# Kernel tuning notes

Measured on AMD Instinct MI355X. Metric: run time of the kernel, lower is better.

## Reference

```python
import jax, jax.numpy as jnp
import numpy as np

SIZE, NC, BITS = 16, 3, 8
NV = NC * BITS * SIZE * SIZE  # 6144
NH = NV
N = 32
K_LS = 32   # fixed cap on T=0 local-search Gibbs sweeps (converged rows are fixed points)
K_CP = 16   # fixed cap on coupling MH iterations (converged rows masked out)


def float2bit(x, bits=BITS):
    # quantize [0,1) floats to `bits` binary planes, as in float2bit(...).flatten(1)
    q = jnp.clip(jnp.floor(x * (2 ** bits)), 0, 2 ** bits - 1).astype(jnp.int32)
    shifts = jnp.arange(bits, dtype=jnp.int32)
    b = (q[..., None] >> shifts) & 1  # [N,nc,H,W,bits]
    return b.astype(jnp.float32)


def energy(params, v, h0, h1):
    W0, W1, b0, b1, b2 = params
    e = -jnp.sum(v * b0, axis=1)
    e = e - jnp.sum(h0 * (v @ W0.T + b1), axis=1)
    e = e - jnp.sum(h1 * (h0 @ W1.T + b2), axis=1)
    return e


def _samp(logits, r, T):
    if T == 0:
        return (logits >= 0).astype(jnp.float32)
    return (r < jax.nn.sigmoid(logits / T)).astype(jnp.float32)


def gibbs_step(params, v, h0, h1, even, fix_v, T, key):
    W0, W1, b0, b1, b2 = params
    if T == 0:
        rv = rh0 = rh1 = None
    else:
        kv, k0, k1 = jax.random.split(key, 3)
        rv = jax.random.uniform(kv, v.shape)
        rh0 = jax.random.uniform(k0, h0.shape)
        rh1 = jax.random.uniform(k1, h1.shape)
    # 'even' sweep order: v -> odd h layers -> even h layers
    v_e = v if fix_v else _samp(h0 @ W0 + b0, rv, T)
    h1_e = _samp(h0 @ W1.T + b2, rh1, T)
    h0_e = _samp(v_e @ W0.T + b1 + h1_e @ W1, rh0, T)
    # 'odd' sweep order: even h layers -> v -> odd h layers
    h0_o = _samp(v @ W0.T + b1 + h1 @ W1, rh0, T)
    v_o = v if fix_v else _samp(h0_o @ W0 + b0, rv, T)
    h1_o = _samp(h0_o @ W1.T + b2, rh1, T)
    m = even[:, None]
    return (jnp.where(m, v_e, v_o), jnp.where(m, h0_e, h0_o), jnp.where(m, h1_e, h1_o))


def local_search(params, v, h0, h1, fix_v, key):
    # T=0 deterministic descent with a fixed per-row even/odd split (rand_u drawn once);
    # converged rows are fixed points of the map, so running a fixed K_LS sweeps over the
    # full batch is equivalent to the torch masked while-loop (up to the iteration cap).
    even = jax.random.uniform(key, (v.shape[0],)) < 0.5
    def body(i, s):
        return gibbs_step(params, s[0], s[1], s[2], even, fix_v, 0, None)
    return jax.lax.fori_loop(0, K_LS, body, (v, h0, h1))


def mh_step(params, v, h0, h1, fix_v, key):
    kv, k0, k1, ku = jax.random.split(key, 4)
    v_p = v if fix_v else (jax.random.uniform(kv, v.shape) < 0.5).astype(jnp.float32)
    h0_p = (jax.random.uniform(k0, h0.shape) < 0.5).astype(jnp.float32)
    h1_p = (jax.random.uniform(k1, h1.shape) < 0.5).astype(jnp.float32)
    log_ratio = energy(params, v, h0, h1) - energy(params, v_p, h0_p, h1_p)
    acc = jax.random.uniform(ku, (v.shape[0],)) < jnp.exp(jnp.minimum(log_ratio, 0.0))
    a = acc[:, None]
    return (v if fix_v else jnp.where(a, v_p, v), jnp.where(a, h0_p, h0), jnp.where(a, h1_p, h1))


def _conv_mask(v_new, h0_new, h1_new, v, h0, h1, fix_v):
    c = jnp.ones(v.shape[0], bool) if fix_v else jnp.all(v_new == v, axis=1)
    return c & jnp.all(h0_new == h0, axis=1) & jnp.all(h1_new == h1, axis=1)


def coupling(params, v, h0, h1, fix_v, key):
    k0, key = jax.random.split(key)
    v1, h01, h11 = mh_step(params, v, h0, h1, fix_v, k0)
    e = energy(params, v1, h01, h11)
    conv = _conv_mask(v1, h01, h11, v, h0, h1, fix_v)
    def body(state, k):
        v, h0, h1, e, conv = state
        v2, h02, h12 = mh_step(params, v, h0, h1, fix_v, k)
        de = energy(params, v2, h02, h12) - energy(params, v, h0, h1)
        m = ~conv
        e = e + jnp.where(m, de, 0.0)
        conv2 = _conv_mask(v2, h02, h12, v, h0, h1, fix_v)
        mm = m[:, None]
        v = jnp.where(mm, v2, v)
        h0 = jnp.where(mm, h02, h0)
        h1 = jnp.where(mm, h12, h1)
        return (v, h0, h1, e, conv | conv2), None
    keys = jax.random.split(key, K_CP)
    (v, h0, h1, e, conv), _ = jax.lax.scan(body, (v1, h01, h11, e, conv), keys)
    return e, v, h0, h1


def _dbm_loss(v_img, W0, W1, b0, b1, b2):
    params = (W0, W1, b0, b1, b2)
    n = v_img.shape[0]
    ks = jax.random.split(jax.random.key(42), 13)
    v = float2bit(v_img).reshape(n, -1)
    # positive phase (visibles clamped, fix_v=True)
    h0 = (jax.random.uniform(ks[0], (n, NH)) < 0.5).astype(jnp.float32)
    h1 = (jax.random.uniform(ks[1], (n, NH)) < 0.5).astype(jnp.float32)
    v, h0, h1 = local_search(params, v, h0, h1, True, ks[2])
    even = jax.random.uniform(ks[3], (n,)) < 0.5
    v, h0, h1 = gibbs_step(params, v, h0, h1, even, True, 1, ks[4])
    e_pos, v, h0, h1 = coupling(params, v, h0, h1, True, ks[5])
    # negative phase (free-running)
    v = (jax.random.uniform(ks[6], v.shape) < 0.5).astype(jnp.float32)
    h0 = (jax.random.uniform(ks[7], (n, NH)) < 0.5).astype(jnp.float32)
    h1 = (jax.random.uniform(ks[8], (n, NH)) < 0.5).astype(jnp.float32)
    v, h0, h1 = local_search(params, v, h0, h1, False, ks[9])
    even = jax.random.uniform(ks[10], (n,)) < 0.5
    v, h0, h1 = gibbs_step(params, v, h0, h1, even, False, 1, ks[11])
    e_neg, v, h0, h1 = coupling(params, v, h0, h1, False, ks[12])
    return e_pos - e_neg  # [N]


def setup_inputs() -> dict:
    key = jax.random.key(0)
    kv, kw0, kw1 = jax.random.split(key, 3)
    v = jax.random.uniform(kv, (N, NC, SIZE, SIZE), dtype=jnp.float32)
    # orthogonal-like scale (unit-norm rows): entries ~ 1/sqrt(fan_in)
    W0 = jax.random.normal(kw0, (NH, NV), dtype=jnp.float32) / np.sqrt(NV)
    W1 = jax.random.normal(kw1, (NH, NH), dtype=jnp.float32) / np.sqrt(NH)
    b0 = jnp.zeros((NV,), jnp.float32)
    b1 = jnp.zeros((NH,), jnp.float32)
    b2 = jnp.zeros((NH,), jnp.float32)
    return {"v": v, "W0": W0, "W1": W1, "b0": b0, "b1": b1, "b2": b2}


def reference(v, W0, W1, b0, b1, b2):
    return _dbm_loss(v, W0, W1, b0, b1, b2)
```

## Files before the change

kernel.cpp:

```cpp
#include <hip/hip_runtime.h>
#include <cstdint>
#include <math.h>

typedef unsigned int u32;
typedef unsigned long long u64;
typedef double d4 __attribute__((ext_vector_type(4)));

#define TF_PARTITIONABLE 1

#define NU 6144
#define NB 32
#define NTOT (NU * NB)
#define NWORD 96
#define NCH 16
#define CHK 384
#define NT_TILES 12
#define HALF_BIG 98304u
#define HALF_SMALL 16u

struct Key { u32 a, b; };
struct UVec { float u[NB]; };

__host__ __device__ __forceinline__ void tf2x32(u32 k0, u32 k1, u32 x0, u32 x1, u32& o0, u32& o1) {
  const u32 k2 = k0 ^ k1 ^ 0x1BD11BDAu;
#define TFR(r) { x0 += x1; x1 = (x1 << r) | (x1 >> (32 - r)); x1 ^= x0; }
  x0 += k0; x1 += k1;
  TFR(13) TFR(15) TFR(26) TFR(6)  x0 += k1; x1 += k2 + 1u;
  TFR(17) TFR(29) TFR(16) TFR(24) x0 += k2; x1 += k0 + 2u;
  TFR(13) TFR(15) TFR(26) TFR(6)  x0 += k0; x1 += k1 + 3u;
  TFR(17) TFR(29) TFR(16) TFR(24) x0 += k1; x1 += k2 + 4u;
  TFR(13) TFR(15) TFR(26) TFR(6)  x0 += k2; x1 += k0 + 5u;
#undef TFR
  o0 = x0; o1 = x1;
}

__host__ __device__ __forceinline__ u32 rbits(u32 k0, u32 k1, u32 t, u32 half) {
#if TF_PARTITIONABLE
  (void)half;
  u32 a, b; tf2x32(k0, k1, 0u, t, a, b); return a ^ b;
#else
  u32 a, b;
  if (t < half) { tf2x32(k0, k1, t, half + t, a, b); return a; }
  tf2x32(k0, k1, t - half, t, a, b); return b;
#endif
}

__host__ __device__ __forceinline__ float u01f(u32 bits) {
  union { u32 u; float f; } c; c.u = (bits >> 9) | 0x3f800000u;
  return c.f - 1.0f;
}

__device__ __forceinline__ double pav(int probe, int l) {
  return probe ? (double)(((l * 13 + 5) & 63) + 1) : (double)(l + 1);
}
__device__ __forceinline__ double pbv(int probe, int l) {
  return probe ? (double)(((l * 11 + 2) & 63) + 1) : (double)(((l * 7 + 3) & 63) + 1);
}

__global__ __launch_bounds__(64) void k_calib(int* __restrict__ tbl) {
  int L = threadIdx.x;
  d4 z = {0.0, 0.0, 0.0, 0.0};
  d4 o0 = __builtin_amdgcn_mfma_f64_16x16x4f64(pav(0, L), pbv(0, L), z, 0, 0, 0);
  d4 o1 = __builtin_amdgcn_mfma_f64_16x16x4f64(pav(1, L), pbv(1, L), z, 0, 0, 0);
  int q = L >> 4, m16 = L & 15;
  int best = -1;
  for (int combo = 0; combo < 16; ++combo) {
    int fa = combo & 1, fb = (combo >> 1) & 1, fd = combo >> 2;
    int ok = 1;
    for (int probe = 0; probe < 2; ++probe) {
#pragma unroll
      for (int r = 0; r < 4; ++r) {
        int i, j;
        if (fd == 0)      { j = m16; i = 4 * q + r; }
        else if (fd == 1) { j = m16; i = q + 4 * r; }
        else if (fd == 2) { i = m16; j = 4 * q + r; }
        else              { i = m16; j = q + 4 * r; }
        double pred = 0.0;
#pragma unroll
        for (int k = 0; k < 4; ++k) {
          int la = fa ? (i * 4 + k) : (k * 16 + i);
          int lb = fb ? (j * 4 + k) : (k * 16 + j);
          pred += pav(probe, la) * pbv(probe, lb);
        }
        double obs = probe ? (r == 0 ? o1[0] : r == 1 ? o1[1] : r == 2 ? o1[2] : o1[3])
                           : (r == 0 ? o0[0] : r == 1 ? o0[1] : r == 2 ? o0[2] : o0[3]);
        if (pred != obs) ok = 0;
      }
    }
    if (__all(ok) && best < 0) best = combo;
  }
  int mA = 0, kA = 0, nB = 0, kB = 0, b0_ = 0, bs = 0, j0 = 0, js = 0, okf = 0;
  if (best >= 0) {
    int fa = best & 1, fb = (best >> 1) & 1, fd = best >> 2;
    if (fa) { mA = L >> 2; kA = L & 3; } else { mA = m16; kA = q; }
    if (fb) { nB = L >> 2; kB = L & 3; } else { nB = m16; kB = q; }
    if (fd == 0)      { j0 = m16; js = 0; b0_ = 4 * q; bs = 1; }
    else if (fd == 1) { j0 = m16; js = 0; b0_ = q; bs = 4; }
    else if (fd == 2) { b0_ = m16; bs = 0; j0 = 4 * q; js = 1; }
    else              { b0_ = m16; bs = 0; j0 = q; js = 4; }
    okf = 1;
  }
  int* p = tbl + L * 16;
  p[0] = mA; p[1] = kA; p[2] = nB; p[3] = kB;
  p[4] = b0_; p[5] = bs; p[6] = j0; p[7] = js; p[8] = okf;
}

__global__ void k_init(u32* __restrict__ flag, u32* __restrict__ chg) { *flag = 0u; *chg = 0u; }

__global__ void k_conv(u32* __restrict__ flag, u32* __restrict__ chg) {
  if (*flag == 0u && *chg == 0u) *flag = 1u;
  *chg = 0u;
}

__global__ void k_allconv(const u32* __restrict__ conv, u32* __restrict__ skipc) {
  if (*skipc) return;
  u32 all = 1u;
  for (int b = 0; b < NB; ++b) all &= conv[b];
  if (all) *skipc = 1u;
}

__global__ __launch_bounds__(256) void k_pos_v(const float* __restrict__ vin, u64* __restrict__ pk) {
  int tid = blockIdx.x * 256 + threadIdx.x;
  int b = tid / 768, p = tid % 768;
  float x = vin[tid];
  int q = (int)floorf(x * 256.0f);
  q = q < 0 ? 0 : (q > 255 ? 255 : q);
  ((unsigned char*)pk)[b * 768 + p] = (unsigned char)q;
}

__global__ __launch_bounds__(256) void k_bern(u32 k0, u32 k1, u64* __restrict__ pk) {
  int tid = blockIdx.x * 256 + threadIdx.x;
  bool s = u01f(rbits(k0, k1, (u32)tid, HALF_BIG)) < 0.5f;
  u64 m = __ballot(s);
  if ((threadIdx.x & 63) == 0) pk[tid >> 6] = m;
}

__global__ __launch_bounds__(256) void k_bern3(u32 has_v, u32 va, u32 vb, u32 ha0, u32 hb0,
                                               u32 ha1, u32 hb1,
                                               u64* __restrict__ pkv, u64* __restrict__ pkh0,
                                               u64* __restrict__ pkh1, const u32* __restrict__ skip) {
  if (skip && *skip) return;
  int tid = blockIdx.x * 256 + threadIdx.x;
  int lane0 = (threadIdx.x & 63) == 0;
  if (has_v) {
    bool s = u01f(rbits(va, vb, (u32)tid, HALF_BIG)) < 0.5f;
    u64 m = __ballot(s);
    if (lane0) pkv[tid >> 6] = m;
  }
  { bool s = u01f(rbits(ha0, hb0, (u32)tid, HALF_BIG)) < 0.5f;
    u64 m = __ballot(s);
    if (lane0) pkh0[tid >> 6] = m; }
  { bool s = u01f(rbits(ha1, hb1, (u32)tid, HALF_BIG)) < 0.5f;
    u64 m = __ballot(s);
    if (lane0) pkh1[tid >> 6] = m; }
}

__device__ __forceinline__ bool samp_dec(float f, int t1, u32 k0, u32 k1, u32 tid) {
  if (t1) {
    double u = (double)u01f(rbits(k0, k1, tid, HALF_BIG));
    return u < 1.0 / (1.0 + exp(-(double)f));
  }
  return f >= 0.0f;
}

__global__ __launch_bounds__(256) void k_samp(const float* __restrict__ fE, const float* __restrict__ fO,
                                              u32 even, int t1, u32 k0, u32 k1,
                                              u64* __restrict__ pk,
                                              const u32* __restrict__ skip, u32* __restrict__ chg) {
  if (skip && *skip) return;
  int tid = blockIdx.x * 256 + threadIdx.x;
  int b = tid / NU;
  float f = ((even >> b) & 1u) ? fE[tid] : fO[tid];
  bool s = samp_dec(f, t1, k0, k1, (u32)tid);
  u64 m = __ballot(s);
  if ((threadIdx.x & 63) == 0) {
    int widx = tid >> 6;
    if (chg) { u64 old = pk[widx]; if (old != m) *chg = 1u; }
    pk[widx] = m;
  }
}

__global__ __launch_bounds__(256) void k_gemm_n(const float* __restrict__ W, const u64* __restrict__ pkx,
                                                double* __restrict__ part, const u32* __restrict__ skip,
                                                const int* __restrict__ tbl) {
  if (skip && *skip) return;
  __shared__ double smem_d[2560];
  int jt = blockIdx.x % 96, c = blockIdx.x / 96;
  int wid = threadIdx.x >> 6, lane = threadIdx.x & 63;
  int kbase = c * CHK;
  int jn0 = jt * 64;
  const int* tp = tbl + lane * 16;
  int okf = tp[8];
  if (okf) {
    float* lw = (float*)smem_d;
    int mA = tp[0], kA = tp[1], nB = tp[2], kB = tp[3];
    int bD0 = tp[4], bDs = tp[5], jD0 = tp[6], jDs = tp[7];
    int t256 = threadIdx.x;
    d4 acc0 = {0.0, 0.0, 0.0, 0.0};
    d4 acc1 = {0.0, 0.0, 0.0, 0.0};
#pragma unroll
    for (int r = 0; r < 2; ++r) {
      int idx = r * 256 + t256, kk = idx >> 4, qq = idx & 15;
      float4 w4 = *(const float4*)(W + (size_t)(kbase + kk) * NU + jn0 + 4 * qq);
      float* d = &lw[kk * 80 + 4 * qq];
      d[0] = w4.x; d[1] = w4.y; d[2] = w4.z; d[3] = w4.w;
    }
    __syncthreads();
    const u64* pxr0 = pkx + (size_t)mA * NWORD + (kbase >> 6);
    const u64* pxr1 = pkx + (size_t)(mA + 16) * NWORD + (kbase >> 6);
    int buf = 0;
    for (int t = 0; t < NT_TILES; ++t) {
      float4 w0p, w1p;
      bool pf = (t + 1) < NT_TILES;
      if (pf) {
        int k0n = kbase + (t + 1) * 32;
        { int idx = t256,       kk = idx >> 4, qq = idx & 15;
          w0p = *(const float4*)(W + (size_t)(k0n + kk) * NU + jn0 + 4 * qq); }
        { int idx = 256 + t256, kk = idx >> 4, qq = idx & 15;
          w1p = *(const float4*)(W + (size_t)(k0n + kk) * NU + jn0 + 4 * qq); }
      }
      u64 ww0 = pxr0[t >> 1], ww1 = pxr1[t >> 1];
      u32 sh = ((u32)(t & 1) << 5) + (u32)kA;
      u32 bb0 = (u32)(ww0 >> sh), bb1 = (u32)(ww1 >> sh);
      const float* lwp = &lw[(buf * 32 + kB) * 80 + wid * 16 + nB];
#pragma unroll
      for (int u = 0; u < 8; ++u) {
        double a0 = (double)((bb0 >> (4 * u)) & 1u);
        double a1 = (double)((bb1 >> (4 * u)) & 1u);
        double wv = (double)lwp[320 * u];
        acc0 = __builtin_amdgcn_mfma_f64_16x16x4f64(a0, wv, acc0, 0, 0, 0);
        acc1 = __builtin_amdgcn_mfma_f64_16x16x4f64(a1, wv, acc1, 0, 0, 0);
      }
      if (pf) {
        int nb = buf ^ 1;
        { int idx = t256,       kk = idx >> 4, qq = idx & 15;
          float* d = &lw[(nb * 32 + kk) * 80 + 4 * qq];
          d[0] = w0p.x; d[1] = w0p.y; d[2] = w0p.z; d[3] = w0p.w; }
        { int idx = 256 + t256, kk = idx >> 4, qq = idx & 15;
          float* d = &lw[(nb * 32 + kk) * 80 + 4 * qq];
          d[0] = w1p.x; d[1] = w1p.y; d[2] = w1p.z; d[3] = w1p.w; }
      }
      __syncthreads();
      buf ^= 1;
    }
    int jn = jn0 + wid * 16;
    double* pp = part + (size_t)c * NTOT + jn;
#pragma unroll
    for (int r = 0; r < 4; ++r) {
      int bi = bD0 + bDs * r, jj = jD0 + jDs * r;
      pp[(size_t)bi * NU + jj] = acc0[r];
      pp[(size_t)(bi + 16) * NU + jj] = acc1[r];
    }
  } else {
    double* red = smem_d;
    int j = jn0 + lane;
    int i0 = kbase + wid * (CHK / 4);
    const float* wp = W + (size_t)i0 * NU + j;
    double acc[32];
#pragma unroll
    for (int b = 0; b < 32; ++b) acc[b] = 0.0;
    for (int i = 0; i < CHK / 4; ++i) {
      double w = (double)wp[(size_t)i * NU];
      int k = i0 + i;
#pragma unroll
      for (int b = 0; b < 32; ++b) {
        double xb = (double)((pkx[(size_t)b * NWORD + (k >> 6)] >> (k & 63)) & 1ull);
        acc[b] = fma(xb, w, acc[b]);
      }
    }
    for (int w = 1; w < 4; ++w) {
      if (wid == w) {
#pragma unroll
        for (int b = 0; b < 32; ++b) red[b * 64 + lane] = acc[b];
      }
      __syncthreads();
      if (wid == 0) {
#pragma unroll
        for (int b = 0; b < 32; ++b) acc[b] += red[b * 64 + lane];
      }
      __syncthreads();
    }
    if (wid == 0) {
      double* pp = part + (size_t)c * NTOT + j;
#pragma unroll
      for (int b = 0; b < 32; ++b) pp[(size_t)b * NU] = acc[b];
    }
  }
}

__global__ __launch_bounds__(256) void k_gemm_t(const float* __restrict__ W, const u64* __restrict__ pkx,
                                                double* __restrict__ part, const u32* __restrict__ skip,
                                                const int* __restrict__ tbl) {
  if (skip && *skip) return;
  __shared__ double smem_d[2176];
  int jt = blockIdx.x % 96, c = blockIdx.x / 96;
  int wid = threadIdx.x >> 6, lane = threadIdx.x & 63;
  int kbase = c * CHK;
  int jn0 = jt * 64;
  const int* tp = tbl + lane * 16;
  int okf = tp[8];
  if (okf) {
    float* lw = (float*)smem_d;
    int mA = tp[0], kA = tp[1], nB = tp[2], kB = tp[3];
    int bD0 = tp[4], bDs = tp[5], jD0 = tp[6], jDs = tp[7];
    int t256 = threadIdx.x;
    d4 acc0 = {0.0, 0.0, 0.0, 0.0};
    d4 acc1 = {0.0, 0.0, 0.0, 0.0};
#pragma unroll
    for (int r = 0; r < 2; ++r) {
      int idx = r * 256 + t256, jj = idx >> 3, kq = idx & 7;
      float4 w4 = *(const float4*)(W + (size_t)(jn0 + jj) * NU + kbase + 4 * kq);
      float* d = &lw[jj * 34 + 4 * kq];
      d[0] = w4.x; d[1] = w4.y; d[2] = w4.z; d[3] = w4.w;
    }
    __syncthreads();
    const u64* pxr0 = pkx + (size_t)mA * NWORD + (kbase >> 6);
    const u64* pxr1 = pkx + (size_t)(mA + 16) * NWORD + (kbase >> 6);
    int buf = 0;
    for (int t = 0; t < NT_TILES; ++t) {
      float4 w0p, w1p;
      bool pf = (t + 1) < NT_TILES;
      if (pf) {
        int k0n = kbase + (t + 1) * 32;
        { int idx = t256,       jj = idx >> 3, kq = idx & 7;
          w0p = *(const float4*)(W + (size_t)(jn0 + jj) * NU + k0n + 4 * kq); }
        { int idx = 256 + t256, jj = idx >> 3, kq = idx & 7;
          w1p = *(const float4*)(W + (size_t)(jn0 + jj) * NU + k0n + 4 * kq); }
      }
      u64 ww0 = pxr0[t >> 1], ww1 = pxr1[t >> 1];
      u32 sh = ((u32)(t & 1) << 5) + (u32)kA;
      u32 bb0 = (u32)(ww0 >> sh), bb1 = (u32)(ww1 >> sh);
      const float* lwp = &lw[(buf * 64 + wid * 16 + nB) * 34 + kB];
#pragma unroll
      for (int u = 0; u < 8; ++u) {
        double a0 = (double)((bb0 >> (4 * u)) & 1u);
        double a1 = (double)((bb1 >> (4 * u)) & 1u);
        double wv = (double)lwp[4 * u];
        acc0 = __builtin_amdgcn_mfma_f64_16x16x4f64(a0, wv, acc0, 0, 0, 0);
        acc1 = __builtin_amdgcn_mfma_f64_16x16x4f64(a1, wv, acc1, 0, 0, 0);
      }
      if (pf) {
        int nb = buf ^ 1;
        { int idx = t256,       jj = idx >> 3, kq = idx & 7;
          float* d = &lw[(nb * 64 + jj) * 34 + 4 * kq];
          d[0] = w0p.x; d[1] = w0p.y; d[2] = w0p.z; d[3] = w0p.w; }
        { int idx = 256 + t256, jj = idx >> 3, kq = idx & 7;
          float* d = &lw[(nb * 64 + jj) * 34 + 4 * kq];
          d[0] = w1p.x; d[1] = w1p.y; d[2] = w1p.z; d[3] = w1p.w; }
      }
      __syncthreads();
      buf ^= 1;
    }
    int jn = jn0 + wid * 16;
    double* pp = part + (size_t)c * NTOT + jn;
#pragma unroll
    for (int r = 0; r < 4; ++r) {
      int bi = bD0 + bDs * r, jj = jD0 + jDs * r;
      pp[(size_t)bi * NU + jj] = acc0[r];
      pp[(size_t)(bi + 16) * NU + jj] = acc1[r];
    }
  } else {
    float* lwf = (float*)smem_d;
    double* red = smem_d;
    int qf = threadIdx.x & 7, af = threadIdx.x >> 3;
    double acc[32];
#pragma unroll
    for (int b = 0; b < 32; ++b) acc[b] = 0.0;
    for (int s = 0; s < NT_TILES; ++s) {
      int ib = kbase + s * 32;
#pragma unroll
      for (int pass = 0; pass < 2; ++pass) {
        int r = pass * 32 + af;
        float4 w4 = *(const float4*)(W + (size_t)(jn0 + r) * NU + ib + qf * 4);
        lwf[(qf * 4 + 0) * 65 + r] = w4.x;
        lwf[(qf * 4 + 1) * 65 + r] = w4.y;
        lwf[(qf * 4 + 2) * 65 + r] = w4.z;
        lwf[(qf * 4 + 3) * 65 + r] = w4.w;
      }
      __syncthreads();
      int iw = wid * 8;
      for (int ii = 0; ii < 8; ++ii) {
        double w = (double)lwf[(iw + ii) * 65 + lane];
        int k = ib + iw + ii;
#pragma unroll
        for (int b = 0; b < 32; ++b) {
          double xb = (double)((pkx[(size_t)b * NWORD + (k >> 6)] >> (k & 63)) & 1ull);
          acc[b] = fma(xb, w, acc[b]);
        }
      }
      __syncthreads();
    }
    for (int w = 1; w < 4; ++w) {
      if (wid == w) {
#pragma unroll
        for (int b = 0; b < 32; ++b) red[b * 64 + lane] = acc[b];
      }
      __syncthreads();
      if (wid == 0) {
#pragma unroll
        for (int b = 0; b < 32; ++b) acc[b] += red[b * 64 + lane];
      }
      __syncthreads();
    }
    if (wid == 0) {
      double* pp = part + (size_t)c * NTOT + jn0 + lane;
#pragma unroll
      for (int b = 0; b < 32; ++b) pp[(size_t)b * NU] = acc[b];
    }
  }
}

__global__ __launch_bounds__(256) void k_reduce(const double* __restrict__ part, const float* __restrict__ bias,
                                                const float* __restrict__ src, float* __restrict__ out,
                                                const u32* __restrict__ skip) {
  if (skip && *skip) return;
  int tid = blockIdx.x * 256 + threadIdx.x;
  int j = tid % NU;
  double s = src ? (double)src[tid] : 0.0;
  if (bias) s += (double)bias[j];
#pragma unroll
  for (int c = 0; c < NCH; ++c) s += part[(size_t)c * NTOT + tid];
  out[tid] = (float)s;
}

__global__ __launch_bounds__(256) void k_redsamp(const double* __restrict__ part, const float* __restrict__ bias,
                                                 const float* __restrict__ src, float* __restrict__ out,
                                                 int t1, u32 k0, u32 k1,
                                                 u64* __restrict__ pk,
                                                 const u32* __restrict__ skip, u32 wmask,
                                                 u32* __restrict__ chg) {
  if (skip && *skip) return;
  int tid = blockIdx.x * 256 + threadIdx.x;
  int j = tid % NU, b = tid / NU;
  double s = src ? (double)src[tid] : 0.0;
  if (bias) s += (double)bias[j];
#pragma unroll
  for (int c = 0; c < NCH; ++c) s += part[(size_t)c * NTOT + tid];
  float f = (float)s;
  if (out) out[tid] = f;
  bool wr = (wmask >> b) & 1u;
  bool smp = samp_dec(f, t1, k0, k1, (u32)tid);
  u64 m = __ballot(smp);
  if (((threadIdx.x & 63) == 0) && wr) {
    int widx = tid >> 6;
    if (chg) { u64 old = pk[widx]; if (old != m) *chg = 1u; }
    pk[widx] = m;
  }
  (void)j;
}

__global__ __launch_bounds__(256) void k_energy(const u64* __restrict__ pkv, const u64* __restrict__ pkh0,
                                                const u64* __restrict__ pkh1, const float* __restrict__ f1,
                                                const float* __restrict__ f2, const float* __restrict__ b0,
                                                float* __restrict__ eout, const u32* __restrict__ skip) {
  if (skip && *skip) return;
  __shared__ double red[256];
  int b = blockIdx.x, t = threadIdx.x;
  double s = 0.0;
  for (int j = t; j < NU; j += 256) {
    int w = j >> 6, bit = j & 63;
    if ((pkv [b * NWORD + w] >> bit) & 1ull) s += (double)b0[j];
    if ((pkh0[b * NWORD + w] >> bit) & 1ull) s += (double)f1[(size_t)b * NU + j];
    if ((pkh1[b * NWORD + w] >> bit) & 1ull) s += (double)f2[(size_t)b * NU + j];
  }
  red[t] = s; __syncthreads();
  for (int off = 128; off > 0; off >>= 1) { if (t < off) red[t] += red[t + off]; __syncthreads(); }
  if (t == 0) eout[b] = (float)(-red[0]);
}

__global__ __launch_bounds__(64) void k_accept(float* __restrict__ ecur, const float* __restrict__ eprop,
                                               float* __restrict__ erun, u32* __restrict__ conv,
                                               u32* __restrict__ accf,
                                               const u64* __restrict__ pv, const u64* __restrict__ pcv,
                                               const u64* __restrict__ ph0, const u64* __restrict__ pch0,
                                               const u64* __restrict__ ph1, const u64* __restrict__ pch1,
                                               UVec uv, int first, const u32* __restrict__ skip) {
  if (skip && *skip) return;
  int b = blockIdx.x, t = threadIdx.x;
  u64 diff = 0ull;
  for (int w = t; w < NWORD; w += 64) {
    size_t o = (size_t)b * NWORD + w;
    if (pv) diff |= pv[o] ^ pcv[o];
    diff |= ph0[o] ^ pch0[o];
    diff |= ph1[o] ^ pch1[o];
  }
  int neq = __any(diff != 0ull);
  if (t == 0) {
    float ec = ecur[b], ep = eprop[b];
    bool acc = (double)uv.u[b] < exp(fmin((double)ec - (double)ep, 0.0));
    bool m = first ? true : (conv[b] == 0u);
    bool upd = m && acc;
    if (first) erun[b] = acc ? ep : ec;
    else if (upd) erun[b] += (ep - ec);
    if (upd) ecur[b] = ep;
    u32 c2 = acc ? (neq ? 0u : 1u) : 1u;
    conv[b] = first ? c2 : (conv[b] | c2);
    accf[b] = upd ? 1u : 0u;
  }
}

__global__ __launch_bounds__(256) void k_merge_pk(const u32* __restrict__ accf,
                                                  const u64* __restrict__ pa, u64* __restrict__ ca,
                                                  const u64* __restrict__ pb, u64* __restrict__ cb,
                                                  const u64* __restrict__ pc, u64* __restrict__ cc,
                                                  const u32* __restrict__ skip) {
  if (skip && *skip) return;
  int w = blockIdx.x * 256 + threadIdx.x;
  if (w >= NB * NWORD) return;
  int b = w / NWORD;
  if (accf[b]) {
    ca[w] = pa[w];
    cb[w] = pb[w];
    if (pc) cc[w] = pc[w];
  }
}

__global__ void k_final(const float* __restrict__ ep, const float* __restrict__ en, float* __restrict__ out) {
  int b = threadIdx.x;
  if (b < NB) out[b] = ep[b] - en[b];
}

static void split_keys(Key k, int n, Key* out) {
#if TF_PARTITIONABLE
  for (int i = 0; i < n; ++i) { u32 a, b; tf2x32(k.a, k.b, 0u, (u32)i, a, b); out[i].a = a; out[i].b = b; }
#else
  u32 flat[64];
  for (int i = 0; i < n; ++i) { u32 a, b; tf2x32(k.a, k.b, (u32)i, (u32)(n + i), a, b); flat[i] = a; flat[n + i] = b; }
  for (int i = 0; i < n; ++i) { out[i].a = flat[2 * i]; out[i].b = flat[2 * i + 1]; }
#endif
}
static u32 mask32(Key k) {
  u32 m = 0;
  for (int b = 0; b < NB; ++b)
    if (u01f(rbits(k.a, k.b, (u32)b, HALF_SMALL)) < 0.5f) m |= (1u << b);
  return m;
}

extern "C" void kernel_launch(void* const* d_in, const int* in_sizes, int n_in,
                              void* d_out, int out_size, void* d_ws, size_t ws_size,
                              hipStream_t stream) {
  const float* vin = (const float*)d_in[0];
  const float* W0  = (const float*)d_in[1];
  const float* W1  = (const float*)d_in[2];
  const float* b0  = (const float*)d_in[3];
  const float* b1  = (const float*)d_in[4];
  const float* b2  = (const float*)d_in[5];
  float* outp = (float*)d_out;

  char* ws = (char*)d_ws;
  size_t off = 0;
  auto alloc = [&](size_t bytes) -> void* {
    void* p = ws + off; off += (bytes + 255) & ~(size_t)255; return p;
  };
  enum { SV = 0, SH0, SH1, SVE, SH1E, SH0O, SVP, SH0P, SH1P, NS };
  enum { IV = 0, IA, IB, IC, ID, IE, IF2, NF };
  u64* PK[NS]; float* F[NF];
  for (int f = 0; f < NF; ++f) F[f] = (float*)alloc((size_t)NTOT * 4);
  double* PART = (double*)alloc((size_t)NCH * NTOT * 8);
  for (int s = 0; s < NS; ++s) PK[s] = (u64*)alloc((size_t)NB * NWORD * 8);
  int*   TBL    = (int*)alloc(64 * 16 * 4);
  float* E_CUR  = (float*)alloc(256);
  float* E_PROP = (float*)alloc(256);
  float* E_POS  = (float*)alloc(256);
  float* E_NEG  = (float*)alloc(256);
  u32*   ACC    = (u32*)alloc(256);
  u32*   CONV   = (u32*)alloc(256);
  u32*   FLAG   = (u32*)alloc(256);
  u32*   CHG    = (u32*)alloc(256);
  u32*   SKIPC  = (u32*)alloc(256);
  u32*   DUMMY  = (u32*)alloc(256);
  if (off > ws_size) return;

  Key root{0u, 42u};
  Key ks[13]; split_keys(root, 13, ks);
  const Key KZ{0u, 0u};

  k_calib<<<dim3(1), dim3(64), 0, stream>>>(TBL);

  auto GEMM_T = [&](const float* Wm, int xs, const u32* skip) {
    k_gemm_t<<<dim3(96 * NCH), dim3(256), 0, stream>>>(Wm, PK[xs], PART, skip, TBL);
  };
  auto GEMM_N = [&](const float* Wm, int xs, const u32* skip) {
    k_gemm_n<<<dim3(96 * NCH), dim3(256), 0, stream>>>(Wm, PK[xs], PART, skip, TBL);
  };
  auto RED = [&](const float* bias, const float* src, float* dst, const u32* skip) {
    k_reduce<<<dim3(768), dim3(256), 0, stream>>>(PART, bias, src, dst, skip);
  };
  auto REDS = [&](const float* bias, const float* src, float* dst, int t1, Key k, int sdst,
                  const u32* skip, u32 wm, u32* chg) {
    k_redsamp<<<dim3(768), dim3(256), 0, stream>>>(PART, bias, src, dst, t1, k.a, k.b,
                                                   PK[sdst], skip, wm, chg);
  };
  auto GT = [&](const float* Wm, int xs, const float* bias, const float* src, float* dst, const u32* skip) {
    GEMM_T(Wm, xs, skip); RED(bias, src, dst, skip);
  };
  auto GN = [&](const float* Wm, int xs, const float* bias, const float* src, float* dst, const u32* skip) {
    GEMM_N(Wm, xs, skip); RED(bias, src, dst, skip);
  };
  auto GTS = [&](const float* Wm, int xs, const float* bias, const float* src, float* dst,
                 int t1, Key k, int sdst, const u32* skip) {
    GEMM_T(Wm, xs, skip); REDS(bias, src, dst, t1, k, sdst, skip, ~0u, nullptr);
  };
  auto GNS = [&](const float* Wm, int xs, const float* bias, const float* src, float* dst,
                 int t1, Key k, int sdst, const u32* skip) {
    GEMM_N(Wm, xs, skip); REDS(bias, src, dst, t1, k, sdst, skip, ~0u, nullptr);
  };
  auto SAMP = [&](const float* fE, const float* fO, u32 even, int t1, Key k, int dst,
                  const u32* skip, u32* chg) {
    k_samp<<<dim3(768), dim3(256), 0, stream>>>(fE, fO, even, t1, k.a, k.b, PK[dst], skip, chg);
  };
  auto BERN = [&](Key k, int dst) {
    k_bern<<<dim3(768), dim3(256), 0, stream>>>(k.a, k.b, PK[dst]);
  };
  auto ENERGY = [&](int sv, int sh0, int sh1, const float* f1, const float* f2, float* eo, const u32* skip) {
    k_energy<<<dim3(32), dim3(256), 0, stream>>>(PK[sv], PK[sh0], PK[sh1], f1, f2, b0, eo, skip);
  };

  auto ls_fixv = [&](u32 evm) {
    auto X = [&](u32 wm) {
      GEMM_T(W1, SH0, FLAG);
      REDS(b2, nullptr, nullptr, 0, KZ, SH1, FLAG, wm, CHG);
    };
    auto Y = [&]() {
      GEMM_N(W1, SH1, FLAG);
      REDS(nullptr, F[IV], nullptr, 0, KZ, SH0, FLAG, ~0u, CHG);
    };
    k_init<<<dim3(1), dim3(1), 0, stream>>>(FLAG, CHG);
    X(evm);
    for (int i = 0; i < 31; ++i) {
      Y(); X(~0u);
      k_conv<<<dim3(1), dim3(1), 0, stream>>>(FLAG, CHG);
    }
    Y(); X(~evm);
  };
  auto ls_free = [&](u32 evm) {
    auto X = [&](u32 wm) {
      GEMM_N(W0, SH0, FLAG);
      REDS(b0, nullptr, nullptr, 0, KZ, SV, FLAG, wm, CHG);
      GEMM_T(W1, SH0, FLAG);
      REDS(b2, nullptr, nullptr, 0, KZ, SH1, FLAG, wm, CHG);
    };
    auto Y = [&]() {
      GT(W0, SV, b1, nullptr, F[IC], FLAG);
      GEMM_N(W1, SH1, FLAG);
      REDS(nullptr, F[IC], nullptr, 0, KZ, SH0, FLAG, ~0u, CHG);
    };
    k_init<<<dim3(1), dim3(1), 0, stream>>>(FLAG, CHG);
    X(evm);
    for (int i = 0; i < 31; ++i) {
      Y(); X(~0u);
      k_conv<<<dim3(1), dim3(1), 0, stream>>>(FLAG, CHG);
    }
    Y(); X(~evm);
  };

  auto gibbs_fixv = [&](u32 even, Key kh0, Key kh1) {
    GTS(W1, SH0, b2, nullptr, F[IA], 1, kh1, SH1E, nullptr);
    GN(W1, SH1E, nullptr, F[IV], F[IB], nullptr);
    GNS(W1, SH1, nullptr, F[IV], F[IC], 1, kh0, SH0O, nullptr);
    GT(W1, SH0O, b2, nullptr, F[ID], nullptr);
    SAMP(F[IB], F[IC], even, 1, kh0, SH0, nullptr, nullptr);
    SAMP(F[IA], F[ID], even, 1, kh1, SH1, nullptr, nullptr);
  };
  auto gibbs_free = [&](u32 even, Key kv, Key kh0, Key kh1) {
    GNS(W0, SH0, b0, nullptr, F[IE], 1, kv, SVE, nullptr);
    GTS(W1, SH0, b2, nullptr, F[IA], 1, kh1, SH1E, nullptr);
    GT(W0, SVE, b1, nullptr, F[IB], nullptr);
    GN(W1, SH1E, nullptr, F[IB], F[IB], nullptr);
    GT(W0, SV, b1, nullptr, F[IC], nullptr);
    GNS(W1, SH1, nullptr, F[IC], F[IC], 1, kh0, SH0O, nullptr);
    GN(W0, SH0O, b0, nullptr, F[IF2], nullptr);
    GT(W1, SH0O, b2, nullptr, F[ID], nullptr);
    SAMP(F[IE], F[IF2], even, 1, kv, SV, nullptr, nullptr);
    SAMP(F[IB], F[IC], even, 1, kh0, SH0, nullptr, nullptr);
    SAMP(F[IA], F[ID], even, 1, kh1, SH1, nullptr, nullptr);
  };

  auto coupling = [&](bool fixv, Key ck, float* erun) {
    Key top[2]; split_keys(ck, 2, top);
    Key cks[17]; cks[0] = top[0];
    { Key rest[16]; split_keys(top[1], 16, rest); for (int i = 0; i < 16; ++i) cks[i + 1] = rest[i]; }
    k_init<<<dim3(1), dim3(1), 0, stream>>>(SKIPC, DUMMY);
    for (int it = 0; it < 17; ++it) {
      const u32* sk = (it == 0) ? nullptr : SKIPC;
      Key sub[4]; split_keys(cks[it], 4, sub);
      UVec uv;
      for (int b = 0; b < NB; ++b) uv.u[b] = u01f(rbits(sub[3].a, sub[3].b, (u32)b, HALF_SMALL));
      k_bern3<<<dim3(768), dim3(256), 0, stream>>>(fixv ? 0u : 1u,
          sub[0].a, sub[0].b, sub[1].a, sub[1].b, sub[2].a, sub[2].b,
          PK[SVP], PK[SH0P], PK[SH1P], sk);
      const float* f1;
      if (fixv) f1 = F[IV];
      else { GT(W0, SVP, b1, nullptr, F[IC], sk); f1 = F[IC]; }
      GT(W1, SH0P, b2, nullptr, F[ID], sk);
      ENERGY(fixv ? SV : SVP, SH0P, SH1P, f1, F[ID], E_PROP, sk);
      k_accept<<<dim3(32), dim3(64), 0, stream>>>(E_CUR, E_PROP, erun, CONV, ACC,
          fixv ? nullptr : PK[SVP], fixv ? nullptr : PK[SV],
          PK[SH0P], PK[SH0], PK[SH1P], PK[SH1], uv, it == 0 ? 1 : 0, sk);
      k_merge_pk<<<dim3(12), dim3(256), 0, stream>>>(ACC, PK[SH0P], PK[SH0], PK[SH1P], PK[SH1],
          fixv ? nullptr : PK[SVP], fixv ? nullptr : PK[SV], sk);
      k_allconv<<<dim3(1), dim3(1), 0, stream>>>(CONV, SKIPC);
    }
  };

  k_pos_v<<<dim3(96), dim3(256), 0, stream>>>(vin, PK[SV]);
  BERN(ks[0], SH0);
  BERN(ks[1], SH1);
  GT(W0, SV, b1, nullptr, F[IV], nullptr);
  u32 ev_ls_pos = mask32(ks[2]);
  ls_fixv(ev_ls_pos);
  u32 ev2_pos = mask32(ks[3]);
  Key g4[3]; split_keys(ks[4], 3, g4);
  gibbs_fixv(ev2_pos, g4[1], g4[2]);
  GT(W1, SH0, b2, nullptr, F[ID], nullptr);
  ENERGY(SV, SH0, SH1, F[IV], F[ID], E_CUR, nullptr);
  coupling(true, ks[5], E_POS);

  BERN(ks[6], SV);
  BERN(ks[7], SH0);
  BERN(ks[8], SH1);
  u32 ev_ls_neg = mask32(ks[9]);
  ls_free(ev_ls_neg);
  u32 ev2_neg = mask32(ks[10]);
  Key g11[3]; split_keys(ks[11], 3, g11);
  gibbs_free(ev2_neg, g11[0], g11[1], g11[2]);
  GT(W0, SV, b1, nullptr, F[IB], nullptr);
  GT(W1, SH0, b2, nullptr, F[IA], nullptr);
  ENERGY(SV, SH0, SH1, F[IB], F[IA], E_CUR, nullptr);
  coupling(false, ks[12], E_NEG);

  k_final<<<dim3(1), dim3(64), 0, stream>>>(E_POS, E_NEG, outp);
}
```

Measured before the change: 13.50 ms.

## Detect period-2 cycles in local search and split fallback GEMM batch accumulators

The local-search loop's convergence test is reworked. Instead of tracking per-write changes with atomics-style flags in the sampling kernels, a new kernel snapshots the packed states into alternating save slots after each sweep. When a state repeats two sweeps later, the loop is treated as having reached a fixed point or 2-cycle, and the remaining sweeps are skipped. A fixup kernel restores the correct parity state so the result matches running every iteration. Separately, the fallback GEMM paths accumulate 8 batch rows at a time in four groups instead of 32 at once, which lowers register pressure at the cost of re-reading the weights four times.

```diff
diff --git a/kernel.cpp b/kernel.cpp
--- a/kernel.cpp
+++ b/kernel.cpp
@@ -12,6 +12,7 @@
 #define NB 32
 #define NTOT (NU * NB)
 #define NWORD 96
+#define SW (NB * NWORD)
 #define NCH 16
 #define CHK 384
 #define NT_TILES 12
@@ -105,18 +106,49 @@
   p[4] = b0_; p[5] = bs; p[6] = j0; p[7] = js; p[8] = okf;
 }
 
-__global__ void k_init(u32* __restrict__ flag, u32* __restrict__ chg) { *flag = 0u; *chg = 0u; }
-
-__global__ void k_conv(u32* __restrict__ flag, u32* __restrict__ chg) {
-  if (*flag == 0u && *chg == 0u) *flag = 1u;
-  *chg = 0u;
-}
+__global__ void k_init(u32* __restrict__ a, u32* __restrict__ b) { *a = 0u; *b = 0u; }
 
 __global__ void k_allconv(const u32* __restrict__ conv, u32* __restrict__ skipc) {
   if (*skipc) return;
   u32 all = 1u;
   for (int b = 0; b < NB; ++b) all &= conv[b];
   if (all) *skipc = 1u;
+}
+
+__global__ __launch_bounds__(256) void k_cyc(const u64* __restrict__ s0, const u64* __restrict__ s1,
+                                             const u64* __restrict__ s2, u64* __restrict__ save,
+                                             int slot, int docmp, int rem_odd, int prev_slot,
+                                             u32* __restrict__ flag, u32* __restrict__ fix) {
+  if (*flag) return;
+  __shared__ u32 neq_sh;
+  if (threadIdx.x == 0) neq_sh = 0u;
+  __syncthreads();
+  u64* sp = save + (size_t)slot * (3 * SW);
+  u32 neq = 0;
+  for (int w = threadIdx.x; w < SW; w += 256) {
+    u64 a0 = s0[w]; if (a0 != sp[w]) neq = 1; sp[w] = a0;
+    u64 a1 = s1[w]; if (a1 != sp[SW + w]) neq = 1; sp[SW + w] = a1;
+    if (s2) { u64 a2 = s2[w]; if (a2 != sp[2 * SW + w]) neq = 1; sp[2 * SW + w] = a2; }
+  }
+  if (neq) neq_sh = 1u;
+  __syncthreads();
+  if (threadIdx.x == 0 && docmp && neq_sh == 0u) {
+    *flag = 1u;
+    *fix = rem_odd ? (1u + (u32)prev_slot) : 0u;
+  }
+}
+
+__global__ __launch_bounds__(256) void k_fixup(u64* __restrict__ s0, u64* __restrict__ s1,
+                                               u64* __restrict__ s2, const u64* __restrict__ save,
+                                               const u32* __restrict__ flag, const u32* __restrict__ fix) {
+  if (!*flag || !*fix) return;
+  const u64* sp = save + (size_t)(*fix - 1u) * (3 * SW);
+  int w = blockIdx.x * 256 + threadIdx.x;
+  if (w < SW) {
+    s0[w] = sp[w];
+    s1[w] = sp[SW + w];
+    if (s2) s2[w] = sp[2 * SW + w];
+  }
 }
 
 __global__ __launch_bounds__(256) void k_pos_v(const float* __restrict__ vin, u64* __restrict__ pk) {
@@ -165,19 +197,14 @@
 
 __global__ __launch_bounds__(256) void k_samp(const float* __restrict__ fE, const float* __restrict__ fO,
                                               u32 even, int t1, u32 k0, u32 k1,
-                                              u64* __restrict__ pk,
-                                              const u32* __restrict__ skip, u32* __restrict__ chg) {
+                                              u64* __restrict__ pk, const u32* __restrict__ skip) {
   if (skip && *skip) return;
   int tid = blockIdx.x * 256 + threadIdx.x;
   int b = tid / NU;
   float f = ((even >> b) & 1u) ? fE[tid] : fO[tid];
   bool s = samp_dec(f, t1, k0, k1, (u32)tid);
   u64 m = __ballot(s);
-  if ((threadIdx.x & 63) == 0) {
-    int widx = tid >> 6;
-    if (chg) { u64 old = pk[widx]; if (old != m) *chg = 1u; }
-    pk[widx] = m;
-  }
+  if ((threadIdx.x & 63) == 0) pk[tid >> 6] = m;
 }
 
 __global__ __launch_bounds__(256) void k_gemm_n(const float* __restrict__ W, const u64* __restrict__ pkx,
@@ -256,34 +283,37 @@
     int j = jn0 + lane;
     int i0 = kbase + wid * (CHK / 4);
     const float* wp = W + (size_t)i0 * NU + j;
-    double acc[32];
-#pragma unroll
-    for (int b = 0; b < 32; ++b) acc[b] = 0.0;
-    for (int i = 0; i < CHK / 4; ++i) {
-      double w = (double)wp[(size_t)i * NU];
-      int k = i0 + i;
-#pragma unroll
-      for (int b = 0; b < 32; ++b) {
-        double xb = (double)((pkx[(size_t)b * NWORD + (k >> 6)] >> (k & 63)) & 1ull);
-        acc[b] = fma(xb, w, acc[b]);
-      }
-    }
-    for (int w = 1; w < 4; ++w) {
-      if (wid == w) {
-#pragma unroll
-        for (int b = 0; b < 32; ++b) red[b * 64 + lane] = acc[b];
+    for (int g = 0; g < 4; ++g) {
+      double acc[8];
+#pragma unroll
+      for (int b = 0; b < 8; ++b) acc[b] = 0.0;
+      for (int i = 0; i < CHK / 4; ++i) {
+        double w = (double)wp[(size_t)i * NU];
+        int k = i0 + i;
+#pragma unroll
+        for (int b = 0; b < 8; ++b) {
+          double xb = (double)((pkx[(size_t)(g * 8 + b) * NWORD + (k >> 6)] >> (k & 63)) & 1ull);
+          acc[b] = fma(xb, w, acc[b]);
+        }
+      }
+      for (int w2 = 1; w2 < 4; ++w2) {
+        if (wid == w2) {
+#pragma unroll
+          for (int b = 0; b < 8; ++b) red[b * 64 + lane] = acc[b];
+        }
+        __syncthreads();
+        if (wid == 0) {
+#pragma unroll
+          for (int b = 0; b < 8; ++b) acc[b] += red[b * 64 + lane];
+        }
+        __syncthreads();
+      }
+      if (wid == 0) {
+        double* pp = part + (size_t)c * NTOT + j;
+#pragma unroll
+        for (int b = 0; b < 8; ++b) pp[(size_t)(g * 8 + b) * NU] = acc[b];
       }
       __syncthreads();
-      if (wid == 0) {
-#pragma unroll
-        for (int b = 0; b < 32; ++b) acc[b] += red[b * 64 + lane];
-      }
-      __syncthreads();
-    }
-    if (wid == 0) {
-      double* pp = part + (size_t)c * NTOT + j;
-#pragma unroll
-      for (int b = 0; b < 32; ++b) pp[(size_t)b * NU] = acc[b];
     }
   }
 }
@@ -363,49 +393,52 @@
     float* lwf = (float*)smem_d;
     double* red = smem_d;
     int qf = threadIdx.x & 7, af = threadIdx.x >> 3;
-    double acc[32];
-#pragma unroll
-    for (int b = 0; b < 32; ++b) acc[b] = 0.0;
-    for (int s = 0; s < NT_TILES; ++s) {
-      int ib = kbase + s * 32;
-#pragma unroll
-      for (int pass = 0; pass < 2; ++pass) {
-        int r = pass * 32 + af;
-        float4 w4 = *(const float4*)(W + (size_t)(jn0 + r) * NU + ib + qf * 4);
-        lwf[(qf * 4 + 0) * 65 + r] = w4.x;
-        lwf[(qf * 4 + 1) * 65 + r] = w4.y;
-        lwf[(qf * 4 + 2) * 65 + r] = w4.z;
-        lwf[(qf * 4 + 3) * 65 + r] = w4.w;
+    for (int g = 0; g < 4; ++g) {
+      double acc[8];
+#pragma unroll
+      for (int b = 0; b < 8; ++b) acc[b] = 0.0;
+      for (int s = 0; s < NT_TILES; ++s) {
+        int ib = kbase + s * 32;
+#pragma unroll
+        for (int pass = 0; pass < 2; ++pass) {
+          int r = pass * 32 + af;
+          float4 w4 = *(const float4*)(W + (size_t)(jn0 + r) * NU + ib + qf * 4);
+          lwf[(qf * 4 + 0) * 65 + r] = w4.x;
+          lwf[(qf * 4 + 1) * 65 + r] = w4.y;
+          lwf[(qf * 4 + 2) * 65 + r] = w4.z;
+          lwf[(qf * 4 + 3) * 65 + r] = w4.w;
+        }
+        __syncthreads();
+        int iw = wid * 8;
+        for (int ii = 0; ii < 8; ++ii) {
+          double w = (double)lwf[(iw + ii) * 65 + lane];
+          int k = ib + iw + ii;
+#pragma unroll
+          for (int b = 0; b < 8; ++b) {
+            double xb = (double)((pkx[(size_t)(g * 8 + b) * NWORD + (k >> 6)] >> (k & 63)) & 1ull);
+            acc[b] = fma(xb, w, acc[b]);
+          }
+        }
+        __syncthreads();
+      }
+      for (int w2 = 1; w2 < 4; ++w2) {
+        if (wid == w2) {
+#pragma unroll
+          for (int b = 0; b < 8; ++b) red[b * 64 + lane] = acc[b];
+        }
+        __syncthreads();
+        if (wid == 0) {
+#pragma unroll
+          for (int b = 0; b < 8; ++b) acc[b] += red[b * 64 + lane];
+        }
+        __syncthreads();
+      }
+      if (wid == 0) {
+        double* pp = part + (size_t)c * NTOT + jn0 + lane;
+#pragma unroll
+        for (int b = 0; b < 8; ++b) pp[(size_t)(g * 8 + b) * NU] = acc[b];
       }
       __syncthreads();
-      int iw = wid * 8;
-      for (int ii = 0; ii < 8; ++ii) {
-        double w = (double)lwf[(iw + ii) * 65 + lane];
-        int k = ib + iw + ii;
-#pragma unroll
-        for (int b = 0; b < 32; ++b) {
-          double xb = (double)((pkx[(size_t)b * NWORD + (k >> 6)] >> (k & 63)) & 1ull);
-          acc[b] = fma(xb, w, acc[b]);
-        }
-      }
-      __syncthreads();
-    }
-    for (int w = 1; w < 4; ++w) {
-      if (wid == w) {
-#pragma unroll
-        for (int b = 0; b < 32; ++b) red[b * 64 + lane] = acc[b];
-      }
-      __syncthreads();
-      if (wid == 0) {
-#pragma unroll
-        for (int b = 0; b < 32; ++b) acc[b] += red[b * 64 + lane];
-      }
-      __syncthreads();
-    }
-    if (wid == 0) {
-      double* pp = part + (size_t)c * NTOT + jn0 + lane;
-#pragma unroll
-      for (int b = 0; b < 32; ++b) pp[(size_t)b * NU] = acc[b];
     }
   }
 }
@@ -427,8 +460,7 @@
                                                  const float* __restrict__ src, float* __restrict__ out,
                                                  int t1, u32 k0, u32 k1,
                                                  u64* __restrict__ pk,
-                                                 const u32* __restrict__ skip, u32 wmask,
-                                                 u32* __restrict__ chg) {
+                                                 const u32* __restrict__ skip, u32 wmask) {
   if (skip && *skip) return;
   int tid = blockIdx.x * 256 + threadIdx.x;
   int j = tid % NU, b = tid / NU;
@@ -441,11 +473,7 @@
   bool wr = (wmask >> b) & 1u;
   bool smp = samp_dec(f, t1, k0, k1, (u32)tid);
   u64 m = __ballot(smp);
-  if (((threadIdx.x & 63) == 0) && wr) {
-    int widx = tid >> 6;
-    if (chg) { u64 old = pk[widx]; if (old != m) *chg = 1u; }
-    pk[widx] = m;
-  }
+  if (((threadIdx.x & 63) == 0) && wr) pk[tid >> 6] = m;
   (void)j;
 }
 
@@ -558,6 +586,7 @@
   for (int f = 0; f < NF; ++f) F[f] = (float*)alloc((size_t)NTOT * 4);
   double* PART = (double*)alloc((size_t)NCH * NTOT * 8);
   for (int s = 0; s < NS; ++s) PK[s] = (u64*)alloc((size_t)NB * NWORD * 8);
+  u64*   SAVE   = (u64*)alloc((size_t)2 * 3 * SW * 8);
   int*   TBL    = (int*)alloc(64 * 16 * 4);
   float* E_CUR  = (float*)alloc(256);
   float* E_PROP = (float*)alloc(256);
@@ -566,7 +595,7 @@
   u32*   ACC    = (u32*)alloc(256);
   u32*   CONV   = (u32*)alloc(256);
   u32*   FLAG   = (u32*)alloc(256);
-  u32*   CHG    = (u32*)alloc(256);
+  u32*   FIX    = (u32*)alloc(256);
   u32*   SKIPC  = (u32*)alloc(256);
   u32*   DUMMY  = (u32*)alloc(256);
   if (off > ws_size) return;
@@ -587,9 +616,9 @@
     k_reduce<<<dim3(768), dim3(256), 0, stream>>>(PART, bias, src, dst, skip);
   };
   auto REDS = [&](const float* bias, const float* src, float* dst, int t1, Key k, int sdst,
-                  const u32* skip, u32 wm, u32* chg) {
+                  const u32* skip, u32 wm) {
     k_redsamp<<<dim3(768), dim3(256), 0, stream>>>(PART, bias, src, dst, t1, k.a, k.b,
-                                                   PK[sdst], skip, wm, chg);
+                                                   PK[sdst], skip, wm);
   };
   auto GT = [&](const float* Wm, int xs, const float* bias, const float* src, float* dst, const u32* skip) {
     GEMM_T(Wm, xs, skip); RED(bias, src, dst, skip);
@@ -599,15 +628,14 @@
   };
   auto GTS = [&](const float* Wm, int xs, const float* bias, const float* src, float* dst,
                  int t1, Key k, int sdst, const u32* skip) {
-    GEMM_T(Wm, xs, skip); REDS(bias, src, dst, t1, k, sdst, skip, ~0u, nullptr);
+    GEMM_T(Wm, xs, skip); REDS(bias, src, dst, t1, k, sdst, skip, ~0u);
   };
   auto GNS = [&](const float* Wm, int xs, const float* bias, const float* src, float* dst,
                  int t1, Key k, int sdst, const u32* skip) {
-    GEMM_N(Wm, xs, skip); REDS(bias, src, dst, t1, k, sdst, skip, ~0u, nullptr);
-  };
-  auto SAMP = [&](const float* fE, const float* fO, u32 even, int t1, Key k, int dst,
-                  const u32* skip, u32* chg) {
-    k_samp<<<dim3(768), dim3(256), 0, stream>>>(fE, fO, even, t1, k.a, k.b, PK[dst], skip, chg);
+    GEMM_N(Wm, xs, skip); REDS(bias, src, dst, t1, k, sdst, skip, ~0u);
+  };
+  auto SAMP = [&](const float* fE, const float* fO, u32 even, int t1, Key k, int dst) {
+    k_samp<<<dim3(768), dim3(256), 0, stream>>>(fE, fO, even, t1, k.a, k.b, PK[dst], nullptr);
   };
   auto BERN = [&](Key k, int dst) {
     k_bern<<<dim3(768), dim3(256), 0, stream>>>(k.a, k.b, PK[dst]);
@@ -617,41 +645,45 @@
   };
 
   auto ls_fixv = [&](u32 evm) {
-    auto X = [&](u32 wm) {
-      GEMM_T(W1, SH0, FLAG);
-      REDS(b2, nullptr, nullptr, 0, KZ, SH1, FLAG, wm, CHG);
+    auto X = [&](u32 wm, const u32* skip) {
+      GEMM_T(W1, SH0, skip);
+      REDS(b2, nullptr, nullptr, 0, KZ, SH1, skip, wm);
     };
-    auto Y = [&]() {
-      GEMM_N(W1, SH1, FLAG);
-      REDS(nullptr, F[IV], nullptr, 0, KZ, SH0, FLAG, ~0u, CHG);
+    auto Y = [&](const u32* skip) {
+      GEMM_N(W1, SH1, skip);
+      REDS(nullptr, F[IV], nullptr, 0, KZ, SH0, skip, ~0u);
     };
-    k_init<<<dim3(1), dim3(1), 0, stream>>>(FLAG, CHG);
-    X(evm);
-    for (int i = 0; i < 31; ++i) {
-      Y(); X(~0u);
-      k_conv<<<dim3(1), dim3(1), 0, stream>>>(FLAG, CHG);
-    }
-    Y(); X(~evm);
+    k_init<<<dim3(1), dim3(1), 0, stream>>>(FLAG, FIX);
+    X(evm, nullptr);
+    for (int i = 1; i <= 31; ++i) {
+      Y(FLAG); X(~0u, FLAG);
+      k_cyc<<<dim3(1), dim3(256), 0, stream>>>(PK[SH0], PK[SH1], nullptr, SAVE,
+          i & 1, (i >= 3) ? 1 : 0, (31 - i) & 1, (i - 1) & 1, FLAG, FIX);
+    }
+    k_fixup<<<dim3(12), dim3(256), 0, stream>>>(PK[SH0], PK[SH1], nullptr, SAVE, FLAG, FIX);
+    Y(nullptr); X(~evm, nullptr);
   };
   auto ls_free = [&](u32 evm) {
-    auto X = [&](u32 wm) {
-      GEMM_N(W0, SH0, FLAG);
-      REDS(b0, nullptr, nullptr, 0, KZ, SV, FLAG, wm, CHG);
-      GEMM_T(W1, SH0, FLAG);
-      REDS(b2, nullptr, nullptr, 0, KZ, SH1, FLAG, wm, CHG);
+    auto X = [&](u32 wm, const u32* skip) {
+      GEMM_N(W0, SH0, skip);
+      REDS(b0, nullptr, nullptr, 0, KZ, SV, skip, wm);
+      GEMM_T(W1, SH0, skip);
+      REDS(b2, nullptr, nullptr, 0, KZ, SH1, skip, wm);
     };
-    auto Y = [&]() {
-      GT(W0, SV, b1, nullptr, F[IC], FLAG);
-      GEMM_N(W1, SH1, FLAG);
-      REDS(nullptr, F[IC], nullptr, 0, KZ, SH0, FLAG, ~0u, CHG);
+    auto Y = [&](const u32* skip) {
+      GT(W0, SV, b1, nullptr, F[IC], skip);
+      GEMM_N(W1, SH1, skip);
+      REDS(nullptr, F[IC], nullptr, 0, KZ, SH0, skip, ~0u);
     };
-    k_init<<<dim3(1), dim3(1), 0, stream>>>(FLAG, CHG);
-    X(evm);
-    for (int i = 0; i < 31; ++i) {
-      Y(); X(~0u);
-      k_conv<<<dim3(1), dim3(1), 0, stream>>>(FLAG, CHG);
-    }
-    Y(); X(~evm);
+    k_init<<<dim3(1), dim3(1), 0, stream>>>(FLAG, FIX);
+    X(evm, nullptr);
+    for (int i = 1; i <= 31; ++i) {
+      Y(FLAG); X(~0u, FLAG);
+      k_cyc<<<dim3(1), dim3(256), 0, stream>>>(PK[SV], PK[SH0], PK[SH1], SAVE,
+          i & 1, (i >= 3) ? 1 : 0, (31 - i) & 1, (i - 1) & 1, FLAG, FIX);
+    }
+    k_fixup<<<dim3(12), dim3(256), 0, stream>>>(PK[SV], PK[SH0], PK[SH1], SAVE, FLAG, FIX);
+    Y(nullptr); X(~evm, nullptr);
   };
 
   auto gibbs_fixv = [&](u32 even, Key kh0, Key kh1) {
@@ -659,8 +691,8 @@
     GN(W1, SH1E, nullptr, F[IV], F[IB], nullptr);
     GNS(W1, SH1, nullptr, F[IV], F[IC], 1, kh0, SH0O, nullptr);
     GT(W1, SH0O, b2, nullptr, F[ID], nullptr);
-    SAMP(F[IB], F[IC], even, 1, kh0, SH0, nullptr, nullptr);
-    SAMP(F[IA], F[ID], even, 1, kh1, SH1, nullptr, nullptr);
+    SAMP(F[IB], F[IC], even, 1, kh0, SH0);
+    SAMP(F[IA], F[ID], even, 1, kh1, SH1);
   };
   auto gibbs_free = [&](u32 even, Key kv, Key kh0, Key kh1) {
     GNS(W0, SH0, b0, nullptr, F[IE], 1, kv, SVE, nullptr);
@@ -671,9 +703,9 @@
     GNS(W1, SH1, nullptr, F[IC], F[IC], 1, kh0, SH0O, nullptr);
     GN(W0, SH0O, b0, nullptr, F[IF2], nullptr);
     GT(W1, SH0O, b2, nullptr, F[ID], nullptr);
-    SAMP(F[IE], F[IF2], even, 1, kv, SV, nullptr, nullptr);
-    SAMP(F[IB], F[IC], even, 1, kh0, SH0, nullptr, nullptr);
-    SAMP(F[IA], F[ID], even, 1, kh1, SH1, nullptr, nullptr);
+    SAMP(F[IE], F[IF2], even, 1, kv, SV);
+    SAMP(F[IB], F[IC], even, 1, kh0, SH0);
+    SAMP(F[IA], F[ID], even, 1, kh1, SH1);
   };
 
   auto coupling = [&](bool fixv, Key ck, float* erun) {
```

Result: no change. 13.70 ms (+1.5%).
